# Kernel tuning notes

Hardware: AMD Instinct MI355X
Metric: run time of the kernel (lower is better)

Reference implementation:

```python
import jax, jax.numpy as jnp
import numpy as np

NUM_ITERS = 3
EPS_ATTN = 1e-8
LN_EPS = 1e-3  # tf.keras LayerNormalization default epsilon


def layernorm(x, g, b):
    m = jnp.mean(x, axis=-1, keepdims=True)
    v = jnp.var(x, axis=-1, keepdims=True)
    return (x - m) * jax.lax.rsqrt(v + LN_EPS) * g + b


def setup_inputs() -> dict:
    key = jax.random.key(0)
    ks = jax.random.split(key, 20)
    B, N, Din, S, D, H = 64, 4096, 64, 7, 64, 128

    def glorot(k, shape):
        fan_in, fan_out = shape[-2], shape[-1]
        lim = np.sqrt(6.0 / (fan_in + fan_out))
        return jax.random.uniform(k, shape, jnp.float32, -lim, lim)

    return {
        "inputs": jax.random.normal(ks[0], (B, N, Din), jnp.float32),
        "slot_noise": jax.random.normal(ks[1], (B, S, D), jnp.float32),
        "ln_in_g": jnp.ones((Din,), jnp.float32), "ln_in_b": jnp.zeros((Din,), jnp.float32),
        "ln_s_g": jnp.ones((D,), jnp.float32), "ln_s_b": jnp.zeros((D,), jnp.float32),
        "ln_m_g": jnp.ones((D,), jnp.float32), "ln_m_b": jnp.zeros((D,), jnp.float32),
        "Wq": glorot(ks[2], (D, D)),
        "Wk": glorot(ks[3], (Din, D)),
        "Wv": glorot(ks[4], (Din, D)),
        "slots_mu": glorot(ks[5], (1, 1, D)),
        "slots_log_sigma": glorot(ks[6], (1, 1, D)),
        "gru_W": glorot(ks[7], (D, 3 * D)),
        "gru_U": glorot(ks[8], (D, 3 * D)),
        "gru_b": jnp.zeros((2, 3 * D), jnp.float32),  # [input_bias, recurrent_bias] (reset_after=True)
        "W1": glorot(ks[9], (D, H)), "b1": jnp.zeros((H,), jnp.float32),
        "W2": glorot(ks[10], (H, D)), "b2": jnp.zeros((D,), jnp.float32),
    }


def reference(inputs, slot_noise, ln_in_g, ln_in_b, ln_s_g, ln_s_b, ln_m_g, ln_m_b,
              Wq, Wk, Wv, slots_mu, slots_log_sigma, gru_W, gru_U, gru_b,
              W1, b1, W2, b2):
    D = Wq.shape[0]
    x = layernorm(inputs, ln_in_g, ln_in_b)          # [B,N,Din]
    k = x @ Wk                                       # [B,N,D]
    v = x @ Wv                                       # [B,N,D]
    slots = slots_mu + jnp.exp(slots_log_sigma) * slot_noise  # [B,S,D]

    scale = D ** (-0.5)
    for _ in range(NUM_ITERS):
        slots_prev = slots
        s = layernorm(slots, ln_s_g, ln_s_b)
        q = (s @ Wq) * scale                         # [B,S,D]
        logits = jnp.einsum("bnd,bsd->bns", k, q)   # [B,N,S]
        attn = jax.nn.softmax(logits, axis=-1) + EPS_ATTN
        attn = attn / jnp.sum(attn, axis=-2, keepdims=True)  # normalize over inputs N
        updates = jnp.einsum("bns,bnd->bsd", attn, v)        # [B,S,D]
        # GRUCell (Keras v2: reset_after=True, sigmoid recurrent activation)
        mx = updates @ gru_W + gru_b[0]
        mh = slots_prev @ gru_U + gru_b[1]
        xz, xr, xh = jnp.split(mx, 3, axis=-1)
        hz, hr, hh = jnp.split(mh, 3, axis=-1)
        z = jax.nn.sigmoid(xz + hz)
        r = jax.nn.sigmoid(xr + hr)
        hcand = jnp.tanh(xh + r * hh)
        slots = z * slots_prev + (1.0 - z) * hcand
        # MLP with residual
        m = layernorm(slots, ln_m_g, ln_m_b)
        slots = slots + jax.nn.relu(m @ W1 + b1) @ W2 + b2
    return slots
```

## Files before the change

### kernel.cpp

```cpp
#include <hip/hip_runtime.h>
#include <hip/hip_bf16.h>


#define NB 64
#define NN 4096
#define NS 7
#define LN_EPS 1e-3f
#define EPS_ATTN 1e-8f

typedef __attribute__((ext_vector_type(8))) __bf16 bf16x8;
typedef __attribute__((ext_vector_type(8))) unsigned short u16x8;
typedef __attribute__((ext_vector_type(4))) float f32x4;
typedef __attribute__((ext_vector_type(4))) unsigned int u32x4;

__device__ __forceinline__ unsigned short f2bf(float f) {
    unsigned int x = __float_as_uint(f);
    x += 0x7FFFu + ((x >> 16) & 1u);
    return (unsigned short)(x >> 16);
}

__device__ __forceinline__ bf16x8 pack8(float4 a, float4 b) {
    u16x8 r;
    r[0] = f2bf(a.x); r[1] = f2bf(a.y); r[2] = f2bf(a.z); r[3] = f2bf(a.w);
    r[4] = f2bf(b.x); r[5] = f2bf(b.y); r[6] = f2bf(b.z); r[7] = f2bf(b.w);
    return __builtin_bit_cast(bf16x8, r);
}

__global__ __launch_bounds__(64) void prep_kernel(
        const float* __restrict__ Wk, const float* __restrict__ Wv,
        const float* __restrict__ g, const float* __restrict__ bb,
        unsigned short* __restrict__ GkT, unsigned short* __restrict__ GvT,
        float* __restrict__ cgk, float* __restrict__ cbk,
        float* __restrict__ cgv, float* __restrict__ cbv) {
    int j = blockIdx.x & 63, mat = blockIdx.x >> 6, d = threadIdx.x;
    const float* W = mat ? Wv : Wk;
    unsigned short* GT = mat ? GvT : GkT;
    float* cg = mat ? cgv : cgk;
    float* cb = mat ? cbv : cbk;
    float w = W[d * 64 + j];
    float gv = g[d], bv = bb[d];
    GT[j * 64 + d] = f2bf(gv * w);
    float sg = gv * w, sb = bv * w;
#pragma unroll
    for (int off = 1; off < 64; off <<= 1) {
        sg += __shfl_xor(sg, off);
        sb += __shfl_xor(sb, off);
    }
    if (d == 0) { cg[j] = sg; cb[j] = sb; }
}

__global__ void init_slots_kernel(const float* __restrict__ noise, const float* __restrict__ mu,
                                  const float* __restrict__ lsig, float* __restrict__ slots) {
    int idx = blockIdx.x * 256 + threadIdx.x;
    if (idx < NB * NS * 64) {
        int d = idx & 63;
        slots[idx] = mu[d] + __expf(lsig[d]) * noise[idx];
    }
}

__global__ __launch_bounds__(256) void proj_kernel(
        const float* __restrict__ x, const unsigned short* __restrict__ GkT,
        const unsigned short* __restrict__ GvT,
        const float* __restrict__ cgk, const float* __restrict__ cbk,
        const float* __restrict__ cgv, const float* __restrict__ cbv,
        unsigned short* __restrict__ kout, unsigned short* __restrict__ vT) {
    __shared__ __align__(16) unsigned short ktile[128 * 72];
    __shared__ __align__(16) unsigned short vtile[64 * 136];
    int t = threadIdx.x;
    int w = t >> 6, lane = t & 63;
    int h = lane >> 4, rl = lane & 15;
    long base = (long)blockIdx.x * 128;
    int bb = blockIdx.x >> 5;
    int nblk = (blockIdx.x & 31) * 128;
    const float* xr0 = x + (base + w * 16 + rl) * 64 + h * 8;
    const float* xr1 = xr0 + 64 * 64;
    float4 xa[8];
    xa[0] = *(const float4*)(xr0);      xa[1] = *(const float4*)(xr0 + 4);
    xa[2] = *(const float4*)(xr0 + 32); xa[3] = *(const float4*)(xr0 + 36);
    xa[4] = *(const float4*)(xr1);      xa[5] = *(const float4*)(xr1 + 4);
    xa[6] = *(const float4*)(xr1 + 32); xa[7] = *(const float4*)(xr1 + 36);
    float s1a = 0.f, s2a = 0.f, s1b = 0.f, s2b = 0.f;
#pragma unroll
    for (int i = 0; i < 4; ++i) {
        s1a += xa[i].x + xa[i].y + xa[i].z + xa[i].w;
        s2a += xa[i].x * xa[i].x + xa[i].y * xa[i].y + xa[i].z * xa[i].z + xa[i].w * xa[i].w;
        s1b += xa[4 + i].x + xa[4 + i].y + xa[4 + i].z + xa[4 + i].w;
        s2b += xa[4 + i].x * xa[4 + i].x + xa[4 + i].y * xa[4 + i].y + xa[4 + i].z * xa[4 + i].z + xa[4 + i].w * xa[4 + i].w;
    }
    s1a += __shfl_xor(s1a, 16); s2a += __shfl_xor(s2a, 16);
    s1a += __shfl_xor(s1a, 32); s2a += __shfl_xor(s2a, 32);
    s1b += __shfl_xor(s1b, 16); s2b += __shfl_xor(s2b, 16);
    s1b += __shfl_xor(s1b, 32); s2b += __shfl_xor(s2b, 32);
    float m0 = s1a * (1.f / 64.f);
    float i0 = rsqrtf(s2a * (1.f / 64.f) - m0 * m0 + LN_EPS);
    float m1 = s1b * (1.f / 64.f);
    float i1 = rsqrtf(s2b * (1.f / 64.f) - m1 * m1 + LN_EPS);
    bf16x8 a00 = pack8(xa[0], xa[1]), a01 = pack8(xa[2], xa[3]);
    bf16x8 a10 = pack8(xa[4], xa[5]), a11 = pack8(xa[6], xa[7]);
    f32x4 k0a[4], v0a[4], k1a[4], v1a[4];
#pragma unroll
    for (int nt = 0; nt < 4; ++nt) {
        k0a[nt] = (f32x4){0.f, 0.f, 0.f, 0.f}; v0a[nt] = (f32x4){0.f, 0.f, 0.f, 0.f};
        k1a[nt] = (f32x4){0.f, 0.f, 0.f, 0.f}; v1a[nt] = (f32x4){0.f, 0.f, 0.f, 0.f};
    }
#pragma unroll
    for (int nt = 0; nt < 4; ++nt) {
        const unsigned short* gk = GkT + (nt * 16 + rl) * 64 + h * 8;
        const unsigned short* gv = GvT + (nt * 16 + rl) * 64 + h * 8;
        bf16x8 bk0 = *(const bf16x8*)(gk);
        bf16x8 bk1 = *(const bf16x8*)(gk + 32);
        bf16x8 bv0 = *(const bf16x8*)(gv);
        bf16x8 bv1 = *(const bf16x8*)(gv + 32);
        k0a[nt] = __builtin_amdgcn_mfma_f32_16x16x32_bf16(a00, bk0, k0a[nt], 0, 0, 0);
        k0a[nt] = __builtin_amdgcn_mfma_f32_16x16x32_bf16(a01, bk1, k0a[nt], 0, 0, 0);
        v0a[nt] = __builtin_amdgcn_mfma_f32_16x16x32_bf16(a00, bv0, v0a[nt], 0, 0, 0);
        v0a[nt] = __builtin_amdgcn_mfma_f32_16x16x32_bf16(a01, bv1, v0a[nt], 0, 0, 0);
        k1a[nt] = __builtin_amdgcn_mfma_f32_16x16x32_bf16(a10, bk0, k1a[nt], 0, 0, 0);
        k1a[nt] = __builtin_amdgcn_mfma_f32_16x16x32_bf16(a11, bk1, k1a[nt], 0, 0, 0);
        v1a[nt] = __builtin_amdgcn_mfma_f32_16x16x32_bf16(a10, bv0, v1a[nt], 0, 0, 0);
        v1a[nt] = __builtin_amdgcn_mfma_f32_16x16x32_bf16(a11, bv1, v1a[nt], 0, 0, 0);
    }
    float mr0[4], ir0[4], mr1[4], ir1[4];
#pragma unroll
    for (int r = 0; r < 4; ++r) {
        int rlsrc = h * 4 + r;
        mr0[r] = __shfl(m0, rlsrc); ir0[r] = __shfl(i0, rlsrc);
        mr1[r] = __shfl(m1, rlsrc); ir1[r] = __shfl(i1, rlsrc);
    }
#pragma unroll
    for (int nt = 0; nt < 4; ++nt) {
        int j = nt * 16 + rl;
        float cgkj = cgk[j], cbkj = cbk[j], cgvj = cgv[j], cbvj = cbv[j];
        unsigned short vv0[4], vv1[4];
#pragma unroll
        for (int r = 0; r < 4; ++r) {
            int row = w * 16 + h * 4 + r;
            ktile[row * 72 + j] = f2bf(ir0[r] * (k0a[nt][r] - mr0[r] * cgkj) + cbkj);
            ktile[(64 + row) * 72 + j] = f2bf(ir1[r] * (k1a[nt][r] - mr1[r] * cgkj) + cbkj);
            vv0[r] = f2bf(ir0[r] * (v0a[nt][r] - mr0[r] * cgvj) + cbvj);
            vv1[r] = f2bf(ir1[r] * (v1a[nt][r] - mr1[r] * cgvj) + cbvj);
        }
        uint2 p0 = make_uint2((unsigned int)vv0[0] | ((unsigned int)vv0[1] << 16),
                              (unsigned int)vv0[2] | ((unsigned int)vv0[3] << 16));
        uint2 p1 = make_uint2((unsigned int)vv1[0] | ((unsigned int)vv1[1] << 16),
                              (unsigned int)vv1[2] | ((unsigned int)vv1[3] << 16));
        *(uint2*)(&vtile[j * 136 + w * 16 + h * 4]) = p0;
        *(uint2*)(&vtile[j * 136 + 64 + w * 16 + h * 4]) = p1;
    }
    __syncthreads();
#pragma unroll
    for (int i = 0; i < 4; ++i) {
        int flat = (i * 256 + t) * 8;
        int row = flat >> 6, col = flat & 63;
        uint4 kd = *(const uint4*)(&ktile[row * 72 + col]);
        *(uint4*)(kout + (base + row) * 64 + col) = kd;
        int dd = flat >> 7, noff = flat & 127;
        uint4 vd = *(const uint4*)(&vtile[dd * 136 + noff]);
        *(uint4*)(vT + ((long)(bb * 64 + dd)) * NN + nblk + noff) = vd;
    }
}

__global__ __launch_bounds__(64) void slots_pre_kernel(
        const float* __restrict__ slots, const float* __restrict__ Wq,
        const float* __restrict__ lg, const float* __restrict__ lb,
        float* __restrict__ q, float* __restrict__ U, float* __restrict__ Z) {
    __shared__ float sn[64];
    int bs = blockIdx.x, d = threadIdx.x;
    float xv = slots[bs * 64 + d];
    float s1 = xv, s2 = xv * xv;
#pragma unroll
    for (int off = 1; off < 64; off <<= 1) {
        s1 += __shfl_xor(s1, off);
        s2 += __shfl_xor(s2, off);
    }
    float m = s1 * (1.f / 64.f);
    float inv = rsqrtf(s2 * (1.f / 64.f) - m * m + LN_EPS);
    sn[d] = (xv - m) * inv * lg[d] + lb[d];
    __syncthreads();
    float acc = 0.f;
#pragma unroll 8
    for (int i = 0; i < 64; ++i) acc += sn[i] * Wq[i * 64 + d];
    q[bs * 64 + d] = acc * 0.125f;
    U[bs * 64 + d] = 0.f;
    if (d == 0) Z[bs] = 0.f;
}

__global__ __launch_bounds__(256) void attn_kernel(
        const unsigned short* __restrict__ kp, const unsigned short* __restrict__ vtp,
        const float* __restrict__ q, float* __restrict__ U, float* __restrict__ Z) {
    __shared__ __align__(16) char smemraw[38912];
    unsigned short* vtile = (unsigned short*)smemraw;
    unsigned int* plds = (unsigned int*)(smemraw + 33792);
    int t = threadIdx.x;
    int b = blockIdx.x >> 4, blk = blockIdx.x & 15;
    int w = t >> 6, lane = t & 63;
    int h = lane >> 4, c = lane & 15;
#pragma unroll
    for (int i = 0; i < 8; ++i) {
        int flat = (i * 256 + t) * 8;
        int dd = flat >> 8, noff = flat & 255;
        uint4 vv = *(const uint4*)(vtp + ((long)(b * 64 + dd)) * NN + blk * 256 + noff);
        *(uint4*)(&vtile[dd * 264 + noff]) = vv;
    }
    bf16x8 qf0, qf1;
    {
        int cs = (c < 7) ? c : 0;
        const float* qr = q + (b * NS + cs) * 64 + h * 8;
        float4 q0 = *(const float4*)(qr);
        float4 q1 = *(const float4*)(qr + 4);
        float4 q2 = *(const float4*)(qr + 32);
        float4 q3 = *(const float4*)(qr + 36);
        if (c >= 7) {
            q0 = make_float4(0.f, 0.f, 0.f, 0.f); q1 = q0; q2 = q0; q3 = q0;
        }
        qf0 = pack8(q0, q1);
        qf1 = pack8(q2, q3);
    }
    f32x4 pv[4];
#pragma unroll
    for (int i = 0; i < 4; ++i) pv[i] = (f32x4){0.f, 0.f, 0.f, 0.f};
    float zac = 0.f;
    unsigned int* pw = plds + w * 320;
    long rb0 = (long)b * NN + blk * 256 + w * 16;
    __syncthreads();
#pragma unroll
    for (int p = 0; p < 2; ++p) {
#pragma unroll
        for (int sh = 0; sh < 2; ++sh) {
            long rowbase = rb0 + p * 128 + sh * 64;
            const unsigned short* ka = kp + (rowbase + c) * 64 + h * 8;
            bf16x8 a0 = *(const bf16x8*)(ka);
            bf16x8 a1 = *(const bf16x8*)(ka + 32);
            f32x4 lg = (f32x4){0.f, 0.f, 0.f, 0.f};
            lg = __builtin_amdgcn_mfma_f32_16x16x32_bf16(a0, qf0, lg, 0, 0, 0);
            lg = __builtin_amdgcn_mfma_f32_16x16x32_bf16(a1, qf1, lg, 0, 0, 0);
            float av[4];
#pragma unroll
            for (int j = 0; j < 4; ++j) {
                float vl = (c < 7) ? lg[j] : -1e30f;
                float mx = vl;
                mx = fmaxf(mx, __shfl_xor(mx, 1));
                mx = fmaxf(mx, __shfl_xor(mx, 2));
                mx = fmaxf(mx, __shfl_xor(mx, 4));
                mx = fmaxf(mx, __shfl_xor(mx, 8));
                float e = (c < 7) ? __expf(lg[j] - mx) : 0.f;
                float se = e;
                se += __shfl_xor(se, 1);
                se += __shfl_xor(se, 2);
                se += __shfl_xor(se, 4);
                se += __shfl_xor(se, 8);
                float a = (c < 7) ? (__fdividef(e, se) + EPS_ATTN) : 0.f;
                av[j] = a;
                zac += a;
            }
            unsigned int w0 = (unsigned int)f2bf(av[0]) | ((unsigned int)f2bf(av[1]) << 16);
            unsigned int w1 = (unsigned int)f2bf(av[2]) | ((unsigned int)f2bf(av[3]) << 16);
            pw[c * 20 + sh * 8 + 2 * h]     = w0;
            pw[c * 20 + sh * 8 + 2 * h + 1] = w1;
        }
        u32x4 pr = *(u32x4*)(&pw[c * 20 + 4 * h]);
        bf16x8 pa = __builtin_bit_cast(bf16x8, pr);
        int nloc = p * 128 + ((h < 2) ? (w * 16 + 8 * h) : (48 + w * 16 + 8 * h));
#pragma unroll
        for (int tile = 0; tile < 4; ++tile) {
            bf16x8 bv = *(const bf16x8*)(&vtile[(tile * 16 + c) * 264 + nloc]);
            pv[tile] = __builtin_amdgcn_mfma_f32_16x16x32_bf16(pa, bv, pv[tile], 0, 0, 0);
        }
    }
    zac += __shfl_xor(zac, 16);
    zac += __shfl_xor(zac, 32);
    if (h == 0 && c < 7) atomicAdd(Z + b * NS + c, zac);
    __syncthreads();
    float* ured = (float*)smemraw;
    if (h < 2) {
#pragma unroll
        for (int tile = 0; tile < 4; ++tile) {
#pragma unroll
            for (int j = 0; j < 4; ++j) {
                ured[w * 512 + (4 * h + j) * 64 + tile * 16 + c] = pv[tile][j];
            }
        }
    }
    __syncthreads();
    for (int idx = t; idx < NS * 64; idx += 256) {
        float tot = ured[idx] + ured[512 + idx] + ured[1024 + idx] + ured[1536 + idx];
        atomicAdd(U + b * NS * 64 + idx, tot);
    }
}

__global__ __launch_bounds__(512) void slots_post_kernel(
        float* __restrict__ slots, float* __restrict__ U, float* __restrict__ Z,
        const float* __restrict__ gW, const float* __restrict__ gU, const float* __restrict__ gb,
        const float* __restrict__ lmg, const float* __restrict__ lmb,
        const float* __restrict__ W1, const float* __restrict__ b1,
        const float* __restrict__ W2, const float* __restrict__ b2,
        const float* __restrict__ Wq, const float* __restrict__ lsg, const float* __restrict__ lsb,
        float* __restrict__ q, float* __restrict__ outp, int last) {
    __shared__ float up[7][64], hp[7][64], hn[7][64], mm[7][64], sl[7][64], sn[7][64];
    __shared__ float hl[7][128];
    __shared__ float mxs[7][192], mhs[7][192];
    int bq = blockIdx.x;
    int t = threadIdx.x;
    int s = t >> 6, d = t & 63;
    if (t < 448) {
        int bs = bq * 7 + s;
        float zsum = Z[bs];
        up[s][d] = U[bs * 64 + d] / zsum;
        hp[s][d] = slots[bs * 64 + d];
        U[bs * 64 + d] = 0.f;
        if (d == 0) Z[bs] = 0.f;
    }
    __syncthreads();
    if (t < 192) {
        float acc[7];
#pragma unroll
        for (int s2 = 0; s2 < 7; ++s2) acc[s2] = gb[t];
#pragma unroll 4
        for (int i = 0; i < 64; ++i) {
            float wv = gW[i * 192 + t];
#pragma unroll
            for (int s2 = 0; s2 < 7; ++s2) acc[s2] += up[s2][i] * wv;
        }
#pragma unroll
        for (int s2 = 0; s2 < 7; ++s2) mxs[s2][t] = acc[s2];
    } else if (t >= 256 && t < 448) {
        int cc = t - 256;
        float acc[7];
#pragma unroll
        for (int s2 = 0; s2 < 7; ++s2) acc[s2] = gb[192 + cc];
#pragma unroll 4
        for (int i = 0; i < 64; ++i) {
            float wv = gU[i * 192 + cc];
#pragma unroll
            for (int s2 = 0; s2 < 7; ++s2) acc[s2] += hp[s2][i] * wv;
        }
#pragma unroll
        for (int s2 = 0; s2 < 7; ++s2) mhs[s2][cc] = acc[s2];
    }
    __syncthreads();
    if (t < 448) {
        float z = 1.f / (1.f + __expf(-(mxs[s][d] + mhs[s][d])));
        float r = 1.f / (1.f + __expf(-(mxs[s][64 + d] + mhs[s][64 + d])));
        float pre = mxs[s][128 + d] + r * mhs[s][128 + d];
        pre = fminf(fmaxf(pre, -15.f), 15.f);
        float e2 = __expf(2.f * pre);
        float hc = (e2 - 1.f) / (e2 + 1.f);
        float hnew = z * hp[s][d] + (1.f - z) * hc;
        hn[s][d] = hnew;
        float s1 = hnew, s2v = hnew * hnew;
#pragma unroll
        for (int off = 1; off < 64; off <<= 1) { s1 += __shfl_xor(s1, off); s2v += __shfl_xor(s2v, off); }
        float m = s1 * (1.f / 64.f);
        float inv = rsqrtf(s2v * (1.f / 64.f) - m * m + LN_EPS);
        mm[s][d] = (hnew - m) * inv * lmg[d] + lmb[d];
    }
    __syncthreads();
    if (t < 128) {
        float acc[7];
#pragma unroll
        for (int s2 = 0; s2 < 7; ++s2) acc[s2] = b1[t];
#pragma unroll 4
        for (int i = 0; i < 64; ++i) {
            float wv = W1[i * 128 + t];
#pragma unroll
            for (int s2 = 0; s2 < 7; ++s2) acc[s2] += mm[s2][i] * wv;
        }
#pragma unroll
        for (int s2 = 0; s2 < 7; ++s2) hl[s2][t] = fmaxf(acc[s2], 0.f);
    }
    __syncthreads();
    if (t < 64) {
        float acc[7];
#pragma unroll
        for (int s2 = 0; s2 < 7; ++s2) acc[s2] = hn[s2][t] + b2[t];
#pragma unroll 4
        for (int j = 0; j < 128; ++j) {
            float wv = W2[j * 64 + t];
#pragma unroll
            for (int s2 = 0; s2 < 7; ++s2) acc[s2] += hl[s2][j] * wv;
        }
#pragma unroll
        for (int s2 = 0; s2 < 7; ++s2) {
            int bs = bq * 7 + s2;
            slots[bs * 64 + t] = acc[s2];
            if (last) outp[bs * 64 + t] = acc[s2];
            sl[s2][t] = acc[s2];
        }
    }
    __syncthreads();
    if (t < 448) {
        float o = sl[s][d];
        float s1 = o, s2v = o * o;
#pragma unroll
        for (int off = 1; off < 64; off <<= 1) { s1 += __shfl_xor(s1, off); s2v += __shfl_xor(s2v, off); }
        float m = s1 * (1.f / 64.f);
        float inv = rsqrtf(s2v * (1.f / 64.f) - m * m + LN_EPS);
        sn[s][d] = (o - m) * inv * lsg[d] + lsb[d];
    }
    __syncthreads();
    if (t < 448) {
        float acc = 0.f;
#pragma unroll 8
        for (int i = 0; i < 64; ++i) acc += sn[s][i] * Wq[i * 64 + d];
        q[(bq * 7 + s) * 64 + d] = acc * 0.125f;
    }
}

extern "C" void kernel_launch(void* const* d_in, const int* in_sizes, int n_in,
                              void* d_out, int out_size, void* d_ws, size_t ws_size,
                              hipStream_t stream) {
    const float* inputs  = (const float*)d_in[0];
    const float* noise   = (const float*)d_in[1];
    const float* ln_in_g = (const float*)d_in[2];
    const float* ln_in_b = (const float*)d_in[3];
    const float* ln_s_g  = (const float*)d_in[4];
    const float* ln_s_b  = (const float*)d_in[5];
    const float* ln_m_g  = (const float*)d_in[6];
    const float* ln_m_b  = (const float*)d_in[7];
    const float* Wq      = (const float*)d_in[8];
    const float* Wk      = (const float*)d_in[9];
    const float* Wv      = (const float*)d_in[10];
    const float* mu      = (const float*)d_in[11];
    const float* lsig    = (const float*)d_in[12];
    const float* gW      = (const float*)d_in[13];
    const float* gU      = (const float*)d_in[14];
    const float* gb      = (const float*)d_in[15];
    const float* W1      = (const float*)d_in[16];
    const float* b1      = (const float*)d_in[17];
    const float* W2      = (const float*)d_in[18];
    const float* b2      = (const float*)d_in[19];

    char* ws = (char*)d_ws;
    unsigned short* kbuf = (unsigned short*)ws;
    unsigned short* vtbuf = (unsigned short*)(ws + 33554432);
    float* slots = (float*)(ws + 67108864);
    float* qbuf  = (float*)(ws + 67108864 + 114688);
    float* Ubuf  = (float*)(ws + 67108864 + 2 * 114688);
    float* Zbuf  = (float*)(ws + 67108864 + 3 * 114688);
    unsigned short* GkT = (unsigned short*)(ws + 67108864 + 3 * 114688 + 4096);
    unsigned short* GvT = GkT + 4096;
    float* cgk = (float*)(GvT + 4096);
    float* cbk = cgk + 64;
    float* cgv = cbk + 64;
    float* cbv = cgv + 64;

    prep_kernel<<<128, 64, 0, stream>>>(Wk, Wv, ln_in_g, ln_in_b, GkT, GvT, cgk, cbk, cgv, cbv);
    init_slots_kernel<<<112, 256, 0, stream>>>(noise, mu, lsig, slots);
    proj_kernel<<<2048, 256, 0, stream>>>(inputs, GkT, GvT, cgk, cbk, cgv, cbv, kbuf, vtbuf);
    slots_pre_kernel<<<448, 64, 0, stream>>>(slots, Wq, ln_s_g, ln_s_b, qbuf, Ubuf, Zbuf);
    for (int it = 0; it < 3; ++it) {
        attn_kernel<<<1024, 256, 0, stream>>>(kbuf, vtbuf, qbuf, Ubuf, Zbuf);
        slots_post_kernel<<<64, 512, 0, stream>>>(slots, Ubuf, Zbuf, gW, gU, gb,
                                                  ln_m_g, ln_m_b, W1, b1, W2, b2,
                                                  Wq, ln_s_g, ln_s_b, qbuf,
                                                  (float*)d_out, (it == 2) ? 1 : 0);
    }
}
```

Measured before the change: 302.2 us.

## Fuse slot update into attention via last-block counter and merge slot init into projection

Slot initialisation and the first query projection move into the tail of the projection kernel, run by its first 448 blocks. The per-iteration slot post-processing (GRU, MLP, next query) moves into the attention kernel: the last of the 16 blocks per batch, detected with an atomic counter and threadfence, does the update. This cuts the launch count from about 9 to 4 and removes the small serial kernels between iterations. The cost is a long serial tail on one block per batch, plus reliance on atomic ordering for correctness.

Measured after the change: 373.9 us. +23.7%, slower.

```diff
diff --git a/kernel.cpp b/kernel.cpp
--- a/kernel.cpp
+++ b/kernel.cpp
@@ -49,21 +49,18 @@
     if (d == 0) { cg[j] = sg; cb[j] = sb; }
 }
 
-__global__ void init_slots_kernel(const float* __restrict__ noise, const float* __restrict__ mu,
-                                  const float* __restrict__ lsig, float* __restrict__ slots) {
-    int idx = blockIdx.x * 256 + threadIdx.x;
-    if (idx < NB * NS * 64) {
-        int d = idx & 63;
-        slots[idx] = mu[d] + __expf(lsig[d]) * noise[idx];
-    }
-}
-
 __global__ __launch_bounds__(256) void proj_kernel(
         const float* __restrict__ x, const unsigned short* __restrict__ GkT,
         const unsigned short* __restrict__ GvT,
         const float* __restrict__ cgk, const float* __restrict__ cbk,
         const float* __restrict__ cgv, const float* __restrict__ cbv,
-        unsigned short* __restrict__ kout, unsigned short* __restrict__ vT) {
+        unsigned short* __restrict__ kout, unsigned short* __restrict__ vT,
+        const float* __restrict__ noise, const float* __restrict__ mu,
+        const float* __restrict__ lsig,
+        const float* __restrict__ Wq, const float* __restrict__ lsg,
+        const float* __restrict__ lsb,
+        float* __restrict__ slots, float* __restrict__ q,
+        float* __restrict__ U, float* __restrict__ Z, int* __restrict__ cnt) {
     __shared__ __align__(16) unsigned short ktile[128 * 72];
     __shared__ __align__(16) unsigned short vtile[64 * 136];
     int t = threadIdx.x;
@@ -85,7 +82,8 @@
         s1a += xa[i].x + xa[i].y + xa[i].z + xa[i].w;
         s2a += xa[i].x * xa[i].x + xa[i].y * xa[i].y + xa[i].z * xa[i].z + xa[i].w * xa[i].w;
         s1b += xa[4 + i].x + xa[4 + i].y + xa[4 + i].z + xa[4 + i].w;
-        s2b += xa[4 + i].x * xa[4 + i].x + xa[4 + i].y * xa[4 + i].y + xa[4 + i].z * xa[4 + i].z + xa[4 + i].w * xa[4 + i].w;
+        s2b += xa[4 + i].x * xa[4 + i].x + xa[4 + i].y * xa[4 + i].y
+             + xa[4 + i].z * xa[4 + i].z + xa[4 + i].w * xa[4 + i].w;
     }
     s1a += __shfl_xor(s1a, 16); s2a += __shfl_xor(s2a, 16);
     s1a += __shfl_xor(s1a, 32); s2a += __shfl_xor(s2a, 32);
@@ -158,37 +156,50 @@
         uint4 vd = *(const uint4*)(&vtile[dd * 136 + noff]);
         *(uint4*)(vT + ((long)(bb * 64 + dd)) * NN + nblk + noff) = vd;
     }
-}
-
-__global__ __launch_bounds__(64) void slots_pre_kernel(
-        const float* __restrict__ slots, const float* __restrict__ Wq,
-        const float* __restrict__ lg, const float* __restrict__ lb,
-        float* __restrict__ q, float* __restrict__ U, float* __restrict__ Z) {
-    __shared__ float sn[64];
-    int bs = blockIdx.x, d = threadIdx.x;
-    float xv = slots[bs * 64 + d];
-    float s1 = xv, s2 = xv * xv;
-#pragma unroll
-    for (int off = 1; off < 64; off <<= 1) {
-        s1 += __shfl_xor(s1, off);
-        s2 += __shfl_xor(s2, off);
-    }
-    float m = s1 * (1.f / 64.f);
-    float inv = rsqrtf(s2 * (1.f / 64.f) - m * m + LN_EPS);
-    sn[d] = (xv - m) * inv * lg[d] + lb[d];
-    __syncthreads();
-    float acc = 0.f;
+    if (blockIdx.x < 448) {
+        int bs = blockIdx.x;
+        __syncthreads();
+        float* sn = (float*)ktile;
+        if (t < 64) {
+            float xv = mu[t] + __expf(lsig[t]) * noise[bs * 64 + t];
+            slots[bs * 64 + t] = xv;
+            float s1 = xv, s2 = xv * xv;
+#pragma unroll
+            for (int off = 1; off < 64; off <<= 1) {
+                s1 += __shfl_xor(s1, off);
+                s2 += __shfl_xor(s2, off);
+            }
+            float m = s1 * (1.f / 64.f);
+            float inv = rsqrtf(s2 * (1.f / 64.f) - m * m + LN_EPS);
+            sn[t] = (xv - m) * inv * lsg[t] + lsb[t];
+            U[bs * 64 + t] = 0.f;
+            if (t == 0) Z[bs] = 0.f;
+            if (bs < 64 && t == 0) cnt[bs] = 0;
+        }
+        __syncthreads();
+        if (t < 64) {
+            float acc = 0.f;
 #pragma unroll 8
-    for (int i = 0; i < 64; ++i) acc += sn[i] * Wq[i * 64 + d];
-    q[bs * 64 + d] = acc * 0.125f;
-    U[bs * 64 + d] = 0.f;
-    if (d == 0) Z[bs] = 0.f;
-}
-
-__global__ __launch_bounds__(256) void attn_kernel(
+            for (int i = 0; i < 64; ++i) acc += sn[i] * Wq[i * 64 + t];
+            q[bs * 64 + t] = acc * 0.125f;
+        }
+    }
+}
+
+__global__ __launch_bounds__(256) void attn_post_kernel(
         const unsigned short* __restrict__ kp, const unsigned short* __restrict__ vtp,
-        const float* __restrict__ q, float* __restrict__ U, float* __restrict__ Z) {
+        float* __restrict__ q, float* __restrict__ U, float* __restrict__ Z,
+        int* __restrict__ cnt, float* __restrict__ slots,
+        const float* __restrict__ gW, const float* __restrict__ gU,
+        const float* __restrict__ gb,
+        const float* __restrict__ lmg, const float* __restrict__ lmb,
+        const float* __restrict__ W1, const float* __restrict__ b1,
+        const float* __restrict__ W2, const float* __restrict__ b2,
+        const float* __restrict__ Wq, const float* __restrict__ lsg,
+        const float* __restrict__ lsb,
+        float* __restrict__ outp, int last) {
     __shared__ __align__(16) char smemraw[38912];
+    __shared__ int islast;
     unsigned short* vtile = (unsigned short*)smemraw;
     unsigned int* plds = (unsigned int*)(smemraw + 33792);
     int t = threadIdx.x;
@@ -284,125 +295,139 @@
     __syncthreads();
     for (int idx = t; idx < NS * 64; idx += 256) {
         float tot = ured[idx] + ured[512 + idx] + ured[1024 + idx] + ured[1536 + idx];
-        atomicAdd(U + b * NS * 64 + idx, tot);
-    }
-}
-
-__global__ __launch_bounds__(512) void slots_post_kernel(
-        float* __restrict__ slots, float* __restrict__ U, float* __restrict__ Z,
-        const float* __restrict__ gW, const float* __restrict__ gU, const float* __restrict__ gb,
-        const float* __restrict__ lmg, const float* __restrict__ lmb,
-        const float* __restrict__ W1, const float* __restrict__ b1,
-        const float* __restrict__ W2, const float* __restrict__ b2,
-        const float* __restrict__ Wq, const float* __restrict__ lsg, const float* __restrict__ lsb,
-        float* __restrict__ q, float* __restrict__ outp, int last) {
-    __shared__ float up[7][64], hp[7][64], hn[7][64], mm[7][64], sl[7][64], sn[7][64];
-    __shared__ float hl[7][128];
-    __shared__ float mxs[7][192], mhs[7][192];
-    int bq = blockIdx.x;
-    int t = threadIdx.x;
-    int s = t >> 6, d = t & 63;
-    if (t < 448) {
-        int bs = bq * 7 + s;
-        float zsum = Z[bs];
-        up[s][d] = U[bs * 64 + d] / zsum;
-        hp[s][d] = slots[bs * 64 + d];
-        U[bs * 64 + d] = 0.f;
-        if (d == 0) Z[bs] = 0.f;
-    }
+        atomicAdd(&U[b * (NS * 64) + idx], tot);
+    }
+    __syncthreads();
+    if (t == 0) {
+        __threadfence();
+        int old = atomicAdd(&cnt[b], 1);
+        islast = (old == 15) ? 1 : 0;
+    }
+    __syncthreads();
+    if (!islast) return;
+    __threadfence();
+    float* S   = (float*)smemraw;
+    float* up  = S;
+    float* hp  = S + 448;
+    float* hn  = S + 896;
+    float* mxs = S + 1344;
+    float* mhs = S + 2688;
+    float* mm  = S + 4032;
+    float* hl  = S + 4480;
+    float* sl  = S + 5376;
+    float* snv = S + 5824;
+    float* zs  = S + 6272;
+    if (t < NS)
+        zs[t] = __hip_atomic_load(&Z[b * NS + t], __ATOMIC_RELAXED, __HIP_MEMORY_SCOPE_AGENT);
+    for (int idx = t; idx < 448; idx += 256) {
+        up[idx] = __hip_atomic_load(&U[b * 448 + idx], __ATOMIC_RELAXED, __HIP_MEMORY_SCOPE_AGENT);
+        hp[idx] = slots[b * 448 + idx];
+    }
+    __syncthreads();
+    for (int idx = t; idx < 448; idx += 256) {
+        up[idx] /= zs[idx >> 6];
+        U[b * 448 + idx] = 0.f;
+    }
+    if (t < NS) Z[b * NS + t] = 0.f;
+    if (t == 0) cnt[b] = 0;
     __syncthreads();
     if (t < 192) {
-        float acc[7];
-#pragma unroll
-        for (int s2 = 0; s2 < 7; ++s2) acc[s2] = gb[t];
-#pragma unroll 4
+        float ax[7], ah[7];
+#pragma unroll
+        for (int s = 0; s < 7; ++s) { ax[s] = gb[t]; ah[s] = gb[192 + t]; }
         for (int i = 0; i < 64; ++i) {
-            float wv = gW[i * 192 + t];
-#pragma unroll
-            for (int s2 = 0; s2 < 7; ++s2) acc[s2] += up[s2][i] * wv;
-        }
-#pragma unroll
-        for (int s2 = 0; s2 < 7; ++s2) mxs[s2][t] = acc[s2];
-    } else if (t >= 256 && t < 448) {
-        int cc = t - 256;
-        float acc[7];
-#pragma unroll
-        for (int s2 = 0; s2 < 7; ++s2) acc[s2] = gb[192 + cc];
-#pragma unroll 4
-        for (int i = 0; i < 64; ++i) {
-            float wv = gU[i * 192 + cc];
-#pragma unroll
-            for (int s2 = 0; s2 < 7; ++s2) acc[s2] += hp[s2][i] * wv;
-        }
-#pragma unroll
-        for (int s2 = 0; s2 < 7; ++s2) mhs[s2][cc] = acc[s2];
-    }
-    __syncthreads();
-    if (t < 448) {
-        float z = 1.f / (1.f + __expf(-(mxs[s][d] + mhs[s][d])));
-        float r = 1.f / (1.f + __expf(-(mxs[s][64 + d] + mhs[s][64 + d])));
-        float pre = mxs[s][128 + d] + r * mhs[s][128 + d];
-        pre = fminf(fmaxf(pre, -15.f), 15.f);
-        float e2 = __expf(2.f * pre);
-        float hc = (e2 - 1.f) / (e2 + 1.f);
-        float hnew = z * hp[s][d] + (1.f - z) * hc;
-        hn[s][d] = hnew;
-        float s1 = hnew, s2v = hnew * hnew;
-#pragma unroll
-        for (int off = 1; off < 64; off <<= 1) { s1 += __shfl_xor(s1, off); s2v += __shfl_xor(s2v, off); }
-        float m = s1 * (1.f / 64.f);
-        float inv = rsqrtf(s2v * (1.f / 64.f) - m * m + LN_EPS);
-        mm[s][d] = (hnew - m) * inv * lmg[d] + lmb[d];
+            float wx = gW[i * 192 + t], wh = gU[i * 192 + t];
+#pragma unroll
+            for (int s = 0; s < 7; ++s) {
+                ax[s] += up[s * 64 + i] * wx;
+                ah[s] += hp[s * 64 + i] * wh;
+            }
+        }
+#pragma unroll
+        for (int s = 0; s < 7; ++s) { mxs[s * 192 + t] = ax[s]; mhs[s * 192 + t] = ah[s]; }
+    }
+    __syncthreads();
+#pragma unroll
+    for (int pass = 0; pass < 2; ++pass) {
+        int idx = pass * 256 + t;
+        if (idx < 448) {
+            int s = idx >> 6, d = idx & 63;
+            float z = 1.f / (1.f + __expf(-(mxs[s * 192 + d] + mhs[s * 192 + d])));
+            float r = 1.f / (1.f + __expf(-(mxs[s * 192 + 64 + d] + mhs[s * 192 + 64 + d])));
+            float pre = mxs[s * 192 + 128 + d] + r * mhs[s * 192 + 128 + d];
+            pre = fminf(fmaxf(pre, -15.f), 15.f);
+            float e2 = __expf(2.f * pre);
+            float hc = (e2 - 1.f) / (e2 + 1.f);
+            float hnew = z * hp[idx] + (1.f - z) * hc;
+            hn[idx] = hnew;
+            float s1 = hnew, s2 = hnew * hnew;
+#pragma unroll
+            for (int off = 1; off < 64; off <<= 1) {
+                s1 += __shfl_xor(s1, off); s2 += __shfl_xor(s2, off);
+            }
+            float m = s1 * (1.f / 64.f);
+            float inv = rsqrtf(s2 * (1.f / 64.f) - m * m + LN_EPS);
+            mm[idx] = (hnew - m) * inv * lmg[d] + lmb[d];
+        }
     }
     __syncthreads();
     if (t < 128) {
         float acc[7];
 #pragma unroll
-        for (int s2 = 0; s2 < 7; ++s2) acc[s2] = b1[t];
-#pragma unroll 4
+        for (int s = 0; s < 7; ++s) acc[s] = b1[t];
         for (int i = 0; i < 64; ++i) {
             float wv = W1[i * 128 + t];
 #pragma unroll
-            for (int s2 = 0; s2 < 7; ++s2) acc[s2] += mm[s2][i] * wv;
-        }
-#pragma unroll
-        for (int s2 = 0; s2 < 7; ++s2) hl[s2][t] = fmaxf(acc[s2], 0.f);
+            for (int s = 0; s < 7; ++s) acc[s] += mm[s * 64 + i] * wv;
+        }
+#pragma unroll
+        for (int s = 0; s < 7; ++s) hl[s * 128 + t] = fmaxf(acc[s], 0.f);
     }
     __syncthreads();
     if (t < 64) {
-        float acc[7];
-#pragma unroll
-        for (int s2 = 0; s2 < 7; ++s2) acc[s2] = hn[s2][t] + b2[t];
-#pragma unroll 4
+        float o[7];
+#pragma unroll
+        for (int s = 0; s < 7; ++s) o[s] = hn[s * 64 + t] + b2[t];
         for (int j = 0; j < 128; ++j) {
             float wv = W2[j * 64 + t];
 #pragma unroll
-            for (int s2 = 0; s2 < 7; ++s2) acc[s2] += hl[s2][j] * wv;
-        }
-#pragma unroll
-        for (int s2 = 0; s2 < 7; ++s2) {
-            int bs = bq * 7 + s2;
-            slots[bs * 64 + t] = acc[s2];
-            if (last) outp[bs * 64 + t] = acc[s2];
-            sl[s2][t] = acc[s2];
-        }
-    }
-    __syncthreads();
-    if (t < 448) {
-        float o = sl[s][d];
-        float s1 = o, s2v = o * o;
-#pragma unroll
-        for (int off = 1; off < 64; off <<= 1) { s1 += __shfl_xor(s1, off); s2v += __shfl_xor(s2v, off); }
-        float m = s1 * (1.f / 64.f);
-        float inv = rsqrtf(s2v * (1.f / 64.f) - m * m + LN_EPS);
-        sn[s][d] = (o - m) * inv * lsg[d] + lsb[d];
-    }
-    __syncthreads();
-    if (t < 448) {
-        float acc = 0.f;
+            for (int s = 0; s < 7; ++s) o[s] += hl[s * 128 + j] * wv;
+        }
+#pragma unroll
+        for (int s = 0; s < 7; ++s) {
+            sl[s * 64 + t] = o[s];
+            slots[b * 448 + s * 64 + t] = o[s];
+            if (last) outp[b * 448 + s * 64 + t] = o[s];
+        }
+    }
+    __syncthreads();
+#pragma unroll
+    for (int pass = 0; pass < 2; ++pass) {
+        int idx = pass * 256 + t;
+        if (idx < 448) {
+            int d = idx & 63;
+            float o = sl[idx];
+            float s1 = o, s2 = o * o;
+#pragma unroll
+            for (int off = 1; off < 64; off <<= 1) {
+                s1 += __shfl_xor(s1, off); s2 += __shfl_xor(s2, off);
+            }
+            float m = s1 * (1.f / 64.f);
+            float inv = rsqrtf(s2 * (1.f / 64.f) - m * m + LN_EPS);
+            snv[idx] = (o - m) * inv * lsg[d] + lsb[d];
+        }
+    }
+    __syncthreads();
+#pragma unroll
+    for (int pass = 0; pass < 2; ++pass) {
+        int idx = pass * 256 + t;
+        if (idx < 448) {
+            int s = idx >> 6, d = idx & 63;
+            float acc = 0.f;
 #pragma unroll 8
-        for (int i = 0; i < 64; ++i) acc += sn[s][i] * Wq[i * 64 + d];
-        q[(bq * 7 + s) * 64 + d] = acc * 0.125f;
+            for (int i = 0; i < 64; ++i) acc += snv[s * 64 + i] * Wq[i * 64 + d];
+            q[b * 448 + idx] = acc * 0.125f;
+        }
     }
 }
 
@@ -431,7 +456,7 @@
     const float* b2      = (const float*)d_in[19];
 
     char* ws = (char*)d_ws;
-    unsigned short* kbuf = (unsigned short*)ws;
+    unsigned short* kbuf  = (unsigned short*)ws;
     unsigned short* vtbuf = (unsigned short*)(ws + 33554432);
     float* slots = (float*)(ws + 67108864);
     float* qbuf  = (float*)(ws + 67108864 + 114688);
@@ -443,16 +468,17 @@
     float* cbk = cgk + 64;
     float* cgv = cbk + 64;
     float* cbv = cgv + 64;
+    int*   cnt = (int*)(cbv + 64);
+    float* outp = (float*)d_out;
 
     prep_kernel<<<128, 64, 0, stream>>>(Wk, Wv, ln_in_g, ln_in_b, GkT, GvT, cgk, cbk, cgv, cbv);
-    init_slots_kernel<<<112, 256, 0, stream>>>(noise, mu, lsig, slots);
-    proj_kernel<<<2048, 256, 0, stream>>>(inputs, GkT, GvT, cgk, cbk, cgv, cbv, kbuf, vtbuf);
-    slots_pre_kernel<<<448, 64, 0, stream>>>(slots, Wq, ln_s_g, ln_s_b, qbuf, Ubuf, Zbuf);
+    proj_kernel<<<2048, 256, 0, stream>>>(inputs, GkT, GvT, cgk, cbk, cgv, cbv, kbuf, vtbuf,
+                                          noise, mu, lsig, Wq, ln_s_g, ln_s_b,
+                                          slots, qbuf, Ubuf, Zbuf, cnt);
     for (int it = 0; it < 3; ++it) {
-        attn_kernel<<<1024, 256, 0, stream>>>(kbuf, vtbuf, qbuf, Ubuf, Zbuf);
-        slots_post_kernel<<<64, 512, 0, stream>>>(slots, Ubuf, Zbuf, gW, gU, gb,
-                                                  ln_m_g, ln_m_b, W1, b1, W2, b2,
-                                                  Wq, ln_s_g, ln_s_b, qbuf,
-                                                  (float*)d_out, (it == 2) ? 1 : 0);
-    }
-}
+        attn_post_kernel<<<1024, 256, 0, stream>>>(kbuf, vtbuf, qbuf, Ubuf, Zbuf, cnt, slots,
+                                                   gW, gU, gb, ln_m_g, ln_m_b,
+                                                   W1, b1, W2, b2, Wq, ln_s_g, ln_s_b,
+                                                   outp, (it == 2) ? 1 : 0);
+    }
+}
```
